# Performance work log

Measured on AMD Instinct MI355X. Metric: run time of the kernel, lower is better.

Reference implementation:

```python
import jax, jax.numpy as jnp
import numpy as np

LN_EPS = 1e-5

def _layernorm(x, gamma, beta):
    # LayerNorm over last axis
    mu = jnp.mean(x, axis=-1, keepdims=True)
    var = jnp.var(x, axis=-1, keepdims=True)
    return (x - mu) * jax.lax.rsqrt(var + LN_EPS) * gamma + beta

def setup_inputs() -> dict:
    key = jax.random.key(0)
    ks = jax.random.split(key, 5)
    N, M, d, K = 65536, 2048, 256, 512
    return {
        "H_rna": jax.random.normal(ks[0], (N, d), jnp.float32),
        "H_drug": jax.random.normal(ks[1], (M, d), jnp.float32),
        "U": jax.random.normal(ks[2], (d, K), jnp.float32),
        "V": jax.random.normal(ks[3], (K, d), jnp.float32),
        "q": jax.random.normal(ks[4], (K,), jnp.float32),
        "g_rna": jnp.ones((K,), jnp.float32),
        "b_rna": jnp.zeros((K,), jnp.float32),
        "g_drug": jnp.ones((K,), jnp.float32),
        "b_drug": jnp.zeros((K,), jnp.float32),
    }

def reference(H_rna, H_drug, U, V, q, g_rna, b_rna, g_drug, b_drug):
    # RNA branch: the torch code repeats H_rna over num_drug then projects;
    # all num_drug copies are identical, so compute once per RNA row.
    A = jnp.tanh(H_rna @ U)                    # [N, K]
    A = _layernorm(A, g_rna, b_rna)            # LN over K
    A = A * q                                  # elementwise gate
    # Drug branch: tanh(V @ H_drug^T) -> LN over K (applied on transposed view)
    Dp = jnp.tanh(V @ H_drug.T)                # [K, M]
    Dp = _layernorm(Dp.T, g_drug, b_drug).T    # LN over K axis -> [K, M]
    # Attention scores; identical across the repeated num_drug dim, so the
    # softmax+matmul+mean collapses exactly to a single [N, M] softmax.
    S = A @ Dp                                 # [N, M]
    P = jax.nn.softmax(S, axis=-1)             # [N, M]
    return P @ H_drug                          # [N, d]
```

## Files before the change

kernel.cpp:

```cpp
#include <hip/hip_runtime.h>
#include <math.h>

#define LN_EPS 1e-5f

typedef _Float16 h8 __attribute__((ext_vector_type(8)));
typedef _Float16 h4 __attribute__((ext_vector_type(4)));
typedef float f32x4 __attribute__((ext_vector_type(4)));

#define MFMA16(A,B,C) __builtin_amdgcn_mfma_f32_16x16x32_f16(A,B,C,0,0,0)

__device__ __forceinline__ float fast_tanh(float x){
    float e = __expf(2.f*x);
    return 1.f - 2.f/(e+1.f);
}

__global__ __launch_bounds__(512) void dp_kernel(
    const float* __restrict__ V, const float* __restrict__ Hd,
    const float* __restrict__ gd, const float* __restrict__ bd,
    _Float16* __restrict__ dp_pack)
{
    __shared__ float h_sh[4][256];
    __shared__ float red1[4][8];
    __shared__ float red2[4][8];

    const int t  = threadIdx.x;
    const int m0 = blockIdx.x * 4;

    for (int i = t; i < 4 * 256; i += 512)
        ((float*)h_sh)[i] = Hd[(size_t)m0 * 256 + i];
    __syncthreads();

    const int k = t;
    float x0 = 0.f, x1 = 0.f, x2 = 0.f, x3 = 0.f;
    for (int j = 0; j < 256; j += 4) {
        float4 v4 = *(const float4*)(V + (size_t)k * 256 + j);
        x0 += v4.x * h_sh[0][j] + v4.y * h_sh[0][j + 1] + v4.z * h_sh[0][j + 2] + v4.w * h_sh[0][j + 3];
        x1 += v4.x * h_sh[1][j] + v4.y * h_sh[1][j + 1] + v4.z * h_sh[1][j + 2] + v4.w * h_sh[1][j + 3];
        x2 += v4.x * h_sh[2][j] + v4.y * h_sh[2][j + 1] + v4.z * h_sh[2][j + 2] + v4.w * h_sh[2][j + 3];
        x3 += v4.x * h_sh[3][j] + v4.y * h_sh[3][j + 1] + v4.z * h_sh[3][j + 2] + v4.w * h_sh[3][j + 3];
    }
    float th[4];
    th[0] = tanhf(x0); th[1] = tanhf(x1); th[2] = tanhf(x2); th[3] = tanhf(x3);

    float s1[4], s2[4];
#pragma unroll
    for (int mi = 0; mi < 4; ++mi) { s1[mi] = th[mi]; s2[mi] = th[mi] * th[mi]; }
#pragma unroll
    for (int off = 32; off > 0; off >>= 1) {
#pragma unroll
        for (int mi = 0; mi < 4; ++mi) {
            s1[mi] += __shfl_xor(s1[mi], off, 64);
            s2[mi] += __shfl_xor(s2[mi], off, 64);
        }
    }
    const int wave = t >> 6;
    if ((t & 63) == 0) {
#pragma unroll
        for (int mi = 0; mi < 4; ++mi) { red1[mi][wave] = s1[mi]; red2[mi][wave] = s2[mi]; }
    }
    __syncthreads();

    const float gk = gd[k];
    const float bk = bd[k];
#pragma unroll
    for (int mi = 0; mi < 4; ++mi) {
        float sa = 0.f, sb = 0.f;
#pragma unroll
        for (int ww = 0; ww < 8; ++ww) { sa += red1[mi][ww]; sb += red2[mi][ww]; }
        float mu  = sa * (1.f / 512.f);
        float var = sb * (1.f / 512.f) - mu * mu;
        float rs  = rsqrtf(var + LN_EPS);
        float a   = (th[mi] - mu) * rs * gk + bk;
        int m  = m0 + mi;
        int mt = m >> 4, kk = k >> 5, ln = (m & 15) + 16 * ((k >> 3) & 3), j = k & 7;
        dp_pack[(size_t)((mt * 16 + kk) * 64 + ln) * 8 + j] = (_Float16)a;
    }
}

__global__ void pack_hd_kernel(const float* __restrict__ Hd, _Float16* __restrict__ hp)
{
    int m = blockIdx.x, c = threadIdx.x;
    float v = Hd[(size_t)m * 256 + c];
    int nt = c >> 4, kk = m >> 5, ln = (c & 15) + 16 * ((m >> 3) & 3), j = m & 7;
    hp[(size_t)((nt * 64 + kk) * 64 + ln) * 8 + j] = (_Float16)v;
}

__global__ void pack_u_kernel(const float* __restrict__ U,
                              _Float16* __restrict__ uh, _Float16* __restrict__ ul)
{
    int jd = blockIdx.x, n = threadIdx.x;
    float v = U[(size_t)jd * 512 + n];
    _Float16 hi = (_Float16)v;
    _Float16 lo = (_Float16)(v - (float)hi);
    int nt = n >> 4, kd = jd >> 5, ln = (n & 15) + 16 * ((jd >> 3) & 3), jj = jd & 7;
    int idx = ((nt * 8 + kd) * 64 + ln) * 8 + jj;
    uh[idx] = hi; ul[idx] = lo;
}

__global__ __launch_bounds__(512) void attn_kernel(
    const float* __restrict__ Hr, const float* __restrict__ q,
    const float* __restrict__ gr, const float* __restrict__ br,
    const _Float16* __restrict__ u_hi, const _Float16* __restrict__ u_lo,
    const _Float16* __restrict__ dp_pack, const _Float16* __restrict__ hd_pack,
    float* __restrict__ out)
{
    __shared__ __align__(16) _Float16 lds0[32768];
    __shared__ __align__(16) _Float16 p_pack[2][16384];
    __shared__ __align__(16) float stats[2][2][64][8];

    const int t    = threadIdx.x;
    const int w    = t >> 6;
    const int lane = t & 63;
    const int q4   = lane >> 4;
    const int l15  = lane & 15;
    const int blk  = blockIdx.x;

    _Float16* hr_hi  = lds0;
    _Float16* hr_lo  = lds0 + 16384;
    _Float16* a_pack = lds0;

    float gq[4], bq[4];
#pragma unroll
    for (int i = 0; i < 4; ++i) {
        int c = w * 64 + 16 * i + l15;
        gq[i] = gr[c] * q[c];
        bq[i] = br[c] * q[c];
    }

    const float* HrB = Hr + (size_t)blk * 64 * 256;
#pragma unroll
    for (int ii = 0; ii < 8; ++ii) {
        int flat = (t + 512 * ii) * 4;
        int r = flat >> 8, c = flat & 255;
        f32x4 v = __builtin_nontemporal_load((const f32x4*)(HrB + flat));
        int base = (((r >> 4) * 8 + (c >> 5)) * 64 + ((r & 15) + 16 * ((c >> 3) & 3))) * 8 + (c & 7);
        h4 hi, lo;
        hi[0] = (_Float16)v[0]; lo[0] = (_Float16)(v[0] - (float)hi[0]);
        hi[1] = (_Float16)v[1]; lo[1] = (_Float16)(v[1] - (float)hi[1]);
        hi[2] = (_Float16)v[2]; lo[2] = (_Float16)(v[2] - (float)hi[2]);
        hi[3] = (_Float16)v[3]; lo[3] = (_Float16)(v[3] - (float)hi[3]);
        *(h4*)(hr_hi + base) = hi;
        *(h4*)(hr_lo + base) = lo;
    }
    __syncthreads();

    f32x4 x[4][4];
#pragma unroll
    for (int rt = 0; rt < 4; ++rt)
#pragma unroll
        for (int ci = 0; ci < 4; ++ci) x[rt][ci] = (f32x4)(0.f);

#pragma unroll
    for (int kd = 0; kd < 8; ++kd) {
        h8 ah[4], al[4];
#pragma unroll
        for (int rt = 0; rt < 4; ++rt) {
            int idx = ((rt * 8 + kd) * 64 + lane) * 8;
            ah[rt] = *(h8*)(hr_hi + idx);
            al[rt] = *(h8*)(hr_lo + idx);
        }
        h8 bh[4], bl[4];
#pragma unroll
        for (int ci = 0; ci < 4; ++ci) {
            int idx = (((w * 4 + ci) * 8 + kd) * 64 + lane) * 8;
            bh[ci] = *(const h8*)(u_hi + idx);
            bl[ci] = *(const h8*)(u_lo + idx);
        }
#pragma unroll
        for (int rt = 0; rt < 4; ++rt)
#pragma unroll
            for (int ci = 0; ci < 4; ++ci) x[rt][ci] = MFMA16(ah[rt], bh[ci], x[rt][ci]);
#pragma unroll
        for (int rt = 0; rt < 4; ++rt)
#pragma unroll
            for (int ci = 0; ci < 4; ++ci) x[rt][ci] = MFMA16(ah[rt], bl[ci], x[rt][ci]);
#pragma unroll
        for (int rt = 0; rt < 4; ++rt)
#pragma unroll
            for (int ci = 0; ci < 4; ++ci) x[rt][ci] = MFMA16(al[rt], bh[ci], x[rt][ci]);
    }

    float s1[4][4], s2[4][4];
#pragma unroll
    for (int rt = 0; rt < 4; ++rt)
#pragma unroll
        for (int e = 0; e < 4; ++e) { s1[rt][e] = 0.f; s2[rt][e] = 0.f; }
#pragma unroll
    for (int rt = 0; rt < 4; ++rt)
#pragma unroll
        for (int ci = 0; ci < 4; ++ci)
#pragma unroll
            for (int e = 0; e < 4; ++e) {
                float th = fast_tanh(x[rt][ci][e]);
                x[rt][ci][e] = th;
                s1[rt][e] += th;
                s2[rt][e] += th * th;
            }
#pragma unroll
    for (int off = 1; off < 16; off <<= 1)
#pragma unroll
        for (int rt = 0; rt < 4; ++rt)
#pragma unroll
            for (int e = 0; e < 4; ++e) {
                s1[rt][e] += __shfl_xor(s1[rt][e], off, 64);
                s2[rt][e] += __shfl_xor(s2[rt][e], off, 64);
            }
    if (l15 == 0) {
#pragma unroll
        for (int rt = 0; rt < 4; ++rt)
#pragma unroll
            for (int e = 0; e < 4; ++e) {
                int row = rt * 16 + q4 * 4 + e;
                stats[0][0][row][w] = s1[rt][e];
                stats[0][1][row][w] = s2[rt][e];
            }
    }
    __syncthreads();

    float mu[4][4], rs_[4][4];
#pragma unroll
    for (int rt = 0; rt < 4; ++rt)
#pragma unroll
        for (int e = 0; e < 4; ++e) {
            int row = rt * 16 + q4 * 4 + e;
            f32x4 v1 = *(f32x4*)&stats[0][0][row][0];
            f32x4 v1b = *(f32x4*)&stats[0][0][row][4];
            f32x4 v2 = *(f32x4*)&stats[0][1][row][0];
            f32x4 v2b = *(f32x4*)&stats[0][1][row][4];
            float S1 = v1[0] + v1[1] + v1[2] + v1[3] + v1b[0] + v1b[1] + v1b[2] + v1b[3];
            float S2 = v2[0] + v2[1] + v2[2] + v2[3] + v2b[0] + v2b[1] + v2b[2] + v2b[3];
            float m  = S1 * (1.f / 512.f);
            float va = S2 * (1.f / 512.f) - m * m;
            mu[rt][e]  = m;
            rs_[rt][e] = rsqrtf(va + LN_EPS);
        }

#pragma unroll
    for (int rt = 0; rt < 4; ++rt)
#pragma unroll
        for (int ci = 0; ci < 4; ++ci)
#pragma unroll
            for (int e = 0; e < 4; ++e) {
                int mrow = q4 * 4 + e;
                int c = w * 64 + 16 * ci + l15;
                float a = (x[rt][ci][e] - mu[rt][e]) * rs_[rt][e] * gq[ci] + bq[ci];
                a_pack[((rt * 16 + (c >> 5)) * 64 + (mrow + 16 * ((c >> 3) & 3))) * 8 + (c & 7)] =
                    (_Float16)a;
            }
    __syncthreads();

    f32x4 o[4][2];
#pragma unroll
    for (int rt = 0; rt < 4; ++rt)
#pragma unroll
        for (int nc = 0; nc < 2; ++nc) o[rt][nc] = (f32x4)(0.f);
    float mrun[4][4], lrun[4][4];
#pragma unroll
    for (int rt = 0; rt < 4; ++rt)
#pragma unroll
        for (int e = 0; e < 4; ++e) { mrun[rt][e] = -3.0e38f; lrun[rt][e] = 0.f; }

    for (int it = 0; it < 8; ++it) {
        const int pb = it & 1;
        f32x4 s[4][2];
#pragma unroll
        for (int rt = 0; rt < 4; ++rt)
#pragma unroll
            for (int ct = 0; ct < 2; ++ct) s[rt][ct] = (f32x4)(0.f);
#pragma unroll
        for (int kk = 0; kk < 16; ++kk) {
            h8 af[4];
#pragma unroll
            for (int rt = 0; rt < 4; ++rt)
                af[rt] = *(h8*)(a_pack + ((rt * 16 + kk) * 64 + lane) * 8);
            h8 bf[2];
#pragma unroll
            for (int ct = 0; ct < 2; ++ct) {
                int mt = it * 16 + w * 2 + ct;
                bf[ct] = *(const h8*)(dp_pack + (size_t)((mt * 16 + kk) * 64 + lane) * 8);
            }
#pragma unroll
            for (int rt = 0; rt < 4; ++rt)
#pragma unroll
                for (int ct = 0; ct < 2; ++ct) s[rt][ct] = MFMA16(af[rt], bf[ct], s[rt][ct]);
        }

        float pm[4][4];
#pragma unroll
        for (int rt = 0; rt < 4; ++rt)
#pragma unroll
            for (int e = 0; e < 4; ++e)
                pm[rt][e] = fmaxf(s[rt][0][e], s[rt][1][e]);
#pragma unroll
        for (int off = 1; off < 16; off <<= 1)
#pragma unroll
            for (int rt = 0; rt < 4; ++rt)
#pragma unroll
                for (int e = 0; e < 4; ++e)
                    pm[rt][e] = fmaxf(pm[rt][e], __shfl_xor(pm[rt][e], off, 64));
        if (l15 == 0) {
#pragma unroll
            for (int rt = 0; rt < 4; ++rt)
#pragma unroll
                for (int e = 0; e < 4; ++e)
                    stats[pb][0][rt * 16 + q4 * 4 + e][w] = pm[rt][e];
        }
        __syncthreads();

        float alpha[4][4], mnew[4][4], psum[4][4];
#pragma unroll
        for (int rt = 0; rt < 4; ++rt)
#pragma unroll
            for (int e = 0; e < 4; ++e) {
                int row = rt * 16 + q4 * 4 + e;
                f32x4 v = *(f32x4*)&stats[pb][0][row][0];
                f32x4 vb = *(f32x4*)&stats[pb][0][row][4];
                float mn = fmaxf(fmaxf(fmaxf(v[0], v[1]), fmaxf(v[2], v[3])),
                                 fmaxf(fmaxf(vb[0], vb[1]), fmaxf(vb[2], vb[3])));
                mn = fmaxf(mn, mrun[rt][e]);
                alpha[rt][e] = __expf(mrun[rt][e] - mn);
                mnew[rt][e]  = mn;
                psum[rt][e]  = 0.f;
            }
#pragma unroll
        for (int rt = 0; rt < 4; ++rt)
#pragma unroll
            for (int ct = 0; ct < 2; ++ct)
#pragma unroll
                for (int e = 0; e < 4; ++e) {
                    float p = __expf(s[rt][ct][e] - mnew[rt][e]);
                    s[rt][ct][e] = p;
                    psum[rt][e] += p;
                }
#pragma unroll
        for (int off = 1; off < 16; off <<= 1)
#pragma unroll
            for (int rt = 0; rt < 4; ++rt)
#pragma unroll
                for (int e = 0; e < 4; ++e)
                    psum[rt][e] += __shfl_xor(psum[rt][e], off, 64);
        if (l15 == 0) {
#pragma unroll
            for (int rt = 0; rt < 4; ++rt)
#pragma unroll
                for (int e = 0; e < 4; ++e)
                    stats[pb][1][rt * 16 + q4 * 4 + e][w] = psum[rt][e];
        }
#pragma unroll
        for (int rt = 0; rt < 4; ++rt)
#pragma unroll
            for (int ct = 0; ct < 2; ++ct)
#pragma unroll
                for (int e = 0; e < 4; ++e) {
                    int mrow = q4 * 4 + e;
                    int col  = 32 * w + 16 * ct + l15;
                    p_pack[pb][((rt * 8 + (col >> 5)) * 64 + (mrow + 16 * ((col >> 3) & 3))) * 8 + (col & 7)] =
                        (_Float16)s[rt][ct][e];
                }
#pragma unroll
        for (int rt = 0; rt < 4; ++rt)
#pragma unroll
            for (int nc = 0; nc < 2; ++nc)
#pragma unroll
                for (int e = 0; e < 4; ++e) o[rt][nc][e] *= alpha[rt][e];
        __syncthreads();

#pragma unroll
        for (int rt = 0; rt < 4; ++rt)
#pragma unroll
            for (int e = 0; e < 4; ++e) {
                int row = rt * 16 + q4 * 4 + e;
                f32x4 v = *(f32x4*)&stats[pb][1][row][0];
                f32x4 vb = *(f32x4*)&stats[pb][1][row][4];
                lrun[rt][e] = lrun[rt][e] * alpha[rt][e] +
                              (v[0] + v[1] + v[2] + v[3] + vb[0] + vb[1] + vb[2] + vb[3]);
                mrun[rt][e] = mnew[rt][e];
            }

#pragma unroll
        for (int kp = 0; kp < 8; ++kp) {
            h8 pf[4];
#pragma unroll
            for (int rt = 0; rt < 4; ++rt)
                pf[rt] = *(h8*)(&p_pack[pb][((rt * 8 + kp) * 64 + lane) * 8]);
            h8 hf[2];
#pragma unroll
            for (int nc = 0; nc < 2; ++nc) {
                int nt = 2 * w + nc;
                hf[nc] = *(const h8*)(hd_pack + (size_t)((nt * 64 + it * 8 + kp) * 64 + lane) * 8);
            }
#pragma unroll
            for (int rt = 0; rt < 4; ++rt)
#pragma unroll
                for (int nc = 0; nc < 2; ++nc) o[rt][nc] = MFMA16(pf[rt], hf[nc], o[rt][nc]);
        }
    }

    float inv[4][4];
#pragma unroll
    for (int rt = 0; rt < 4; ++rt)
#pragma unroll
        for (int e = 0; e < 4; ++e) inv[rt][e] = 1.f / lrun[rt][e];
#pragma unroll
    for (int rt = 0; rt < 4; ++rt)
#pragma unroll
        for (int nc = 0; nc < 2; ++nc)
#pragma unroll
            for (int e = 0; e < 4; ++e) {
                int row = rt * 16 + q4 * 4 + e;
                int c   = (2 * w + nc) * 16 + l15;
                out[((size_t)blk * 64 + row) * 256 + c] = o[rt][nc][e] * inv[rt][e];
            }
}

extern "C" void kernel_launch(void* const* d_in, const int* in_sizes, int n_in,
                              void* d_out, int out_size, void* d_ws, size_t ws_size,
                              hipStream_t stream)
{
    const float* Hr = (const float*)d_in[0];
    const float* Hd = (const float*)d_in[1];
    const float* U  = (const float*)d_in[2];
    const float* V  = (const float*)d_in[3];
    const float* q  = (const float*)d_in[4];
    const float* gr = (const float*)d_in[5];
    const float* br = (const float*)d_in[6];
    const float* gd = (const float*)d_in[7];
    const float* bd = (const float*)d_in[8];
    float* out = (float*)d_out;

    const int N = in_sizes[0] / 256;
    const int M = in_sizes[1] / 256;

    char* ws = (char*)d_ws;
    _Float16* dp_pack = (_Float16*)ws;
    _Float16* hd_pack = (_Float16*)(ws + (2u << 20));
    _Float16* u_hi    = (_Float16*)(ws + (3u << 20));
    _Float16* u_lo    = (_Float16*)(ws + (3u << 20) + (256u << 10));

    dp_kernel<<<dim3(M / 4), dim3(512), 0, stream>>>(V, Hd, gd, bd, dp_pack);
    pack_hd_kernel<<<dim3(M), dim3(256), 0, stream>>>(Hd, hd_pack);
    pack_u_kernel<<<dim3(256), dim3(512), 0, stream>>>(U, u_hi, u_lo);
    attn_kernel<<<dim3(N / 64), dim3(512), 0, stream>>>(Hr, q, gr, br, u_hi, u_lo,
                                                        dp_pack, hd_pack, out);
}
```

Measured before the change: 688.1 us.

## Give each wave its own row tile in flash attention loop, drop block syncs

Each block now handles 128 RNA rows in two passes of the U projection and LayerNorm stage. In the attention loop each wave owns 16 rows with its A fragments held in registers, streams all drug columns itself and keeps a private P tile in LDS. This removes the per-iteration block-wide max/sum reductions and __syncthreads. It also adds lazy softmax rescaling (rescale only when the running max grows by more than 8) and register double-buffering of dp_pack loads. The cost is more registers (16 output accumulators plus 16 A fragments), more LDS, and each wave reading all of dp_pack and hd_pack from global memory, which lowers operand reuse across waves.

Result: slower. 1.243 ms (+80.7%).

```diff
diff --git a/kernel.cpp b/kernel.cpp
--- a/kernel.cpp
+++ b/kernel.cpp
@@ -104,9 +104,9 @@
     const _Float16* __restrict__ dp_pack, const _Float16* __restrict__ hd_pack,
     float* __restrict__ out)
 {
-    __shared__ __align__(16) _Float16 lds0[32768];
-    __shared__ __align__(16) _Float16 p_pack[2][16384];
-    __shared__ __align__(16) float stats[2][2][64][8];
+    __shared__ __align__(16) _Float16 lds0[65536];
+    __shared__ __align__(16) _Float16 p_lds[8192];
+    __shared__ __align__(16) float stats[2][64][8];
 
     const int t    = threadIdx.x;
     const int w    = t >> 6;
@@ -115,8 +115,8 @@
     const int l15  = lane & 15;
     const int blk  = blockIdx.x;
 
-    _Float16* hr_hi  = lds0;
-    _Float16* hr_lo  = lds0 + 16384;
+    _Float16* hr_hi  = lds0 + 32768;
+    _Float16* hr_lo  = lds0 + 49152;
     _Float16* a_pack = lds0;
 
     float gq[4], bq[4];
@@ -127,290 +127,239 @@
         bq[i] = br[c] * q[c];
     }
 
-    const float* HrB = Hr + (size_t)blk * 64 * 256;
-#pragma unroll
-    for (int ii = 0; ii < 8; ++ii) {
-        int flat = (t + 512 * ii) * 4;
-        int r = flat >> 8, c = flat & 255;
-        f32x4 v = __builtin_nontemporal_load((const f32x4*)(HrB + flat));
-        int base = (((r >> 4) * 8 + (c >> 5)) * 64 + ((r & 15) + 16 * ((c >> 3) & 3))) * 8 + (c & 7);
-        h4 hi, lo;
-        hi[0] = (_Float16)v[0]; lo[0] = (_Float16)(v[0] - (float)hi[0]);
-        hi[1] = (_Float16)v[1]; lo[1] = (_Float16)(v[1] - (float)hi[1]);
-        hi[2] = (_Float16)v[2]; lo[2] = (_Float16)(v[2] - (float)hi[2]);
-        hi[3] = (_Float16)v[3]; lo[3] = (_Float16)(v[3] - (float)hi[3]);
-        *(h4*)(hr_hi + base) = hi;
-        *(h4*)(hr_lo + base) = lo;
-    }
-    __syncthreads();
-
-    f32x4 x[4][4];
-#pragma unroll
-    for (int rt = 0; rt < 4; ++rt)
-#pragma unroll
-        for (int ci = 0; ci < 4; ++ci) x[rt][ci] = (f32x4)(0.f);
-
-#pragma unroll
-    for (int kd = 0; kd < 8; ++kd) {
-        h8 ah[4], al[4];
-#pragma unroll
-        for (int rt = 0; rt < 4; ++rt) {
-            int idx = ((rt * 8 + kd) * 64 + lane) * 8;
-            ah[rt] = *(h8*)(hr_hi + idx);
-            al[rt] = *(h8*)(hr_lo + idx);
-        }
-        h8 bh[4], bl[4];
-#pragma unroll
-        for (int ci = 0; ci < 4; ++ci) {
-            int idx = (((w * 4 + ci) * 8 + kd) * 64 + lane) * 8;
-            bh[ci] = *(const h8*)(u_hi + idx);
-            bl[ci] = *(const h8*)(u_lo + idx);
-        }
-#pragma unroll
-        for (int rt = 0; rt < 4; ++rt)
-#pragma unroll
-            for (int ci = 0; ci < 4; ++ci) x[rt][ci] = MFMA16(ah[rt], bh[ci], x[rt][ci]);
-#pragma unroll
-        for (int rt = 0; rt < 4; ++rt)
-#pragma unroll
-            for (int ci = 0; ci < 4; ++ci) x[rt][ci] = MFMA16(ah[rt], bl[ci], x[rt][ci]);
-#pragma unroll
-        for (int rt = 0; rt < 4; ++rt)
-#pragma unroll
-            for (int ci = 0; ci < 4; ++ci) x[rt][ci] = MFMA16(al[rt], bh[ci], x[rt][ci]);
-    }
-
-    float s1[4][4], s2[4][4];
-#pragma unroll
-    for (int rt = 0; rt < 4; ++rt)
-#pragma unroll
-        for (int e = 0; e < 4; ++e) { s1[rt][e] = 0.f; s2[rt][e] = 0.f; }
-#pragma unroll
-    for (int rt = 0; rt < 4; ++rt)
-#pragma unroll
-        for (int ci = 0; ci < 4; ++ci)
-#pragma unroll
-            for (int e = 0; e < 4; ++e) {
-                float th = fast_tanh(x[rt][ci][e]);
-                x[rt][ci][e] = th;
-                s1[rt][e] += th;
-                s2[rt][e] += th * th;
-            }
-#pragma unroll
-    for (int off = 1; off < 16; off <<= 1)
-#pragma unroll
-        for (int rt = 0; rt < 4; ++rt)
-#pragma unroll
-            for (int e = 0; e < 4; ++e) {
-                s1[rt][e] += __shfl_xor(s1[rt][e], off, 64);
-                s2[rt][e] += __shfl_xor(s2[rt][e], off, 64);
-            }
-    if (l15 == 0) {
+    for (int pass = 0; pass < 2; ++pass) {
+        const float* HrB = Hr + ((size_t)blk * 128 + pass * 64) * 256;
+#pragma unroll
+        for (int ii = 0; ii < 8; ++ii) {
+            int flat = (t + 512 * ii) * 4;
+            int r = flat >> 8, c = flat & 255;
+            f32x4 v = __builtin_nontemporal_load((const f32x4*)(HrB + flat));
+            int base = (((r >> 4) * 8 + (c >> 5)) * 64 + ((r & 15) + 16 * ((c >> 3) & 3))) * 8 + (c & 7);
+            h4 hi, lo;
+            hi[0] = (_Float16)v[0]; lo[0] = (_Float16)(v[0] - (float)hi[0]);
+            hi[1] = (_Float16)v[1]; lo[1] = (_Float16)(v[1] - (float)hi[1]);
+            hi[2] = (_Float16)v[2]; lo[2] = (_Float16)(v[2] - (float)hi[2]);
+            hi[3] = (_Float16)v[3]; lo[3] = (_Float16)(v[3] - (float)hi[3]);
+            *(h4*)(hr_hi + base) = hi;
+            *(h4*)(hr_lo + base) = lo;
+        }
+        __syncthreads();
+
+        f32x4 x[4][4];
+#pragma unroll
+        for (int rt = 0; rt < 4; ++rt)
+#pragma unroll
+            for (int ci = 0; ci < 4; ++ci) x[rt][ci] = (f32x4)(0.f);
+
+#pragma unroll
+        for (int kd = 0; kd < 8; ++kd) {
+            h8 ah[4], al[4];
+#pragma unroll
+            for (int rt = 0; rt < 4; ++rt) {
+                int idx = ((rt * 8 + kd) * 64 + lane) * 8;
+                ah[rt] = *(h8*)(hr_hi + idx);
+                al[rt] = *(h8*)(hr_lo + idx);
+            }
+            h8 bh[4], bl[4];
+#pragma unroll
+            for (int ci = 0; ci < 4; ++ci) {
+                int idx = (((w * 4 + ci) * 8 + kd) * 64 + lane) * 8;
+                bh[ci] = *(const h8*)(u_hi + idx);
+                bl[ci] = *(const h8*)(u_lo + idx);
+            }
+#pragma unroll
+            for (int rt = 0; rt < 4; ++rt)
+#pragma unroll
+                for (int ci = 0; ci < 4; ++ci) x[rt][ci] = MFMA16(ah[rt], bh[ci], x[rt][ci]);
+#pragma unroll
+            for (int rt = 0; rt < 4; ++rt)
+#pragma unroll
+                for (int ci = 0; ci < 4; ++ci) x[rt][ci] = MFMA16(ah[rt], bl[ci], x[rt][ci]);
+#pragma unroll
+            for (int rt = 0; rt < 4; ++rt)
+#pragma unroll
+                for (int ci = 0; ci < 4; ++ci) x[rt][ci] = MFMA16(al[rt], bh[ci], x[rt][ci]);
+        }
+
+        float s1[4][4], s2[4][4];
+#pragma unroll
+        for (int rt = 0; rt < 4; ++rt)
+#pragma unroll
+            for (int e = 0; e < 4; ++e) { s1[rt][e] = 0.f; s2[rt][e] = 0.f; }
+#pragma unroll
+        for (int rt = 0; rt < 4; ++rt)
+#pragma unroll
+            for (int ci = 0; ci < 4; ++ci)
+#pragma unroll
+                for (int e = 0; e < 4; ++e) {
+                    float th = fast_tanh(x[rt][ci][e]);
+                    x[rt][ci][e] = th;
+                    s1[rt][e] += th;
+                    s2[rt][e] += th * th;
+                }
+#pragma unroll
+        for (int off = 1; off < 16; off <<= 1)
+#pragma unroll
+            for (int rt = 0; rt < 4; ++rt)
+#pragma unroll
+                for (int e = 0; e < 4; ++e) {
+                    s1[rt][e] += __shfl_xor(s1[rt][e], off, 64);
+                    s2[rt][e] += __shfl_xor(s2[rt][e], off, 64);
+                }
+        if (l15 == 0) {
+#pragma unroll
+            for (int rt = 0; rt < 4; ++rt)
+#pragma unroll
+                for (int e = 0; e < 4; ++e) {
+                    int row = rt * 16 + q4 * 4 + e;
+                    stats[0][row][w] = s1[rt][e];
+                    stats[1][row][w] = s2[rt][e];
+                }
+        }
+        __syncthreads();
+
+        float mu[4][4], rs_[4][4];
 #pragma unroll
         for (int rt = 0; rt < 4; ++rt)
 #pragma unroll
             for (int e = 0; e < 4; ++e) {
                 int row = rt * 16 + q4 * 4 + e;
-                stats[0][0][row][w] = s1[rt][e];
-                stats[0][1][row][w] = s2[rt][e];
-            }
-    }
-    __syncthreads();
-
-    float mu[4][4], rs_[4][4];
-#pragma unroll
-    for (int rt = 0; rt < 4; ++rt)
-#pragma unroll
-        for (int e = 0; e < 4; ++e) {
-            int row = rt * 16 + q4 * 4 + e;
-            f32x4 v1 = *(f32x4*)&stats[0][0][row][0];
-            f32x4 v1b = *(f32x4*)&stats[0][0][row][4];
-            f32x4 v2 = *(f32x4*)&stats[0][1][row][0];
-            f32x4 v2b = *(f32x4*)&stats[0][1][row][4];
-            float S1 = v1[0] + v1[1] + v1[2] + v1[3] + v1b[0] + v1b[1] + v1b[2] + v1b[3];
-            float S2 = v2[0] + v2[1] + v2[2] + v2[3] + v2b[0] + v2b[1] + v2b[2] + v2b[3];
-            float m  = S1 * (1.f / 512.f);
-            float va = S2 * (1.f / 512.f) - m * m;
-            mu[rt][e]  = m;
-            rs_[rt][e] = rsqrtf(va + LN_EPS);
-        }
-
-#pragma unroll
-    for (int rt = 0; rt < 4; ++rt)
-#pragma unroll
-        for (int ci = 0; ci < 4; ++ci)
-#pragma unroll
-            for (int e = 0; e < 4; ++e) {
-                int mrow = q4 * 4 + e;
-                int c = w * 64 + 16 * ci + l15;
-                float a = (x[rt][ci][e] - mu[rt][e]) * rs_[rt][e] * gq[ci] + bq[ci];
-                a_pack[((rt * 16 + (c >> 5)) * 64 + (mrow + 16 * ((c >> 3) & 3))) * 8 + (c & 7)] =
-                    (_Float16)a;
-            }
-    __syncthreads();
-
-    f32x4 o[4][2];
-#pragma unroll
-    for (int rt = 0; rt < 4; ++rt)
-#pragma unroll
-        for (int nc = 0; nc < 2; ++nc) o[rt][nc] = (f32x4)(0.f);
-    float mrun[4][4], lrun[4][4];
-#pragma unroll
-    for (int rt = 0; rt < 4; ++rt)
-#pragma unroll
-        for (int e = 0; e < 4; ++e) { mrun[rt][e] = -3.0e38f; lrun[rt][e] = 0.f; }
-
-    for (int it = 0; it < 8; ++it) {
-        const int pb = it & 1;
-        f32x4 s[4][2];
-#pragma unroll
-        for (int rt = 0; rt < 4; ++rt)
-#pragma unroll
-            for (int ct = 0; ct < 2; ++ct) s[rt][ct] = (f32x4)(0.f);
-#pragma unroll
-        for (int kk = 0; kk < 16; ++kk) {
-            h8 af[4];
-#pragma unroll
-            for (int rt = 0; rt < 4; ++rt)
-                af[rt] = *(h8*)(a_pack + ((rt * 16 + kk) * 64 + lane) * 8);
-            h8 bf[2];
-#pragma unroll
-            for (int ct = 0; ct < 2; ++ct) {
-                int mt = it * 16 + w * 2 + ct;
-                bf[ct] = *(const h8*)(dp_pack + (size_t)((mt * 16 + kk) * 64 + lane) * 8);
-            }
-#pragma unroll
-            for (int rt = 0; rt < 4; ++rt)
-#pragma unroll
-                for (int ct = 0; ct < 2; ++ct) s[rt][ct] = MFMA16(af[rt], bf[ct], s[rt][ct]);
-        }
-
-        float pm[4][4];
-#pragma unroll
-        for (int rt = 0; rt < 4; ++rt)
-#pragma unroll
-            for (int e = 0; e < 4; ++e)
-                pm[rt][e] = fmaxf(s[rt][0][e], s[rt][1][e]);
-#pragma unroll
-        for (int off = 1; off < 16; off <<= 1)
-#pragma unroll
-            for (int rt = 0; rt < 4; ++rt)
-#pragma unroll
-                for (int e = 0; e < 4; ++e)
-                    pm[rt][e] = fmaxf(pm[rt][e], __shfl_xor(pm[rt][e], off, 64));
-        if (l15 == 0) {
-#pragma unroll
-            for (int rt = 0; rt < 4; ++rt)
-#pragma unroll
-                for (int e = 0; e < 4; ++e)
-                    stats[pb][0][rt * 16 + q4 * 4 + e][w] = pm[rt][e];
-        }
-        __syncthreads();
-
-        float alpha[4][4], mnew[4][4], psum[4][4];
-#pragma unroll
-        for (int rt = 0; rt < 4; ++rt)
-#pragma unroll
-            for (int e = 0; e < 4; ++e) {
-                int row = rt * 16 + q4 * 4 + e;
-                f32x4 v = *(f32x4*)&stats[pb][0][row][0];
-                f32x4 vb = *(f32x4*)&stats[pb][0][row][4];
-                float mn = fmaxf(fmaxf(fmaxf(v[0], v[1]), fmaxf(v[2], v[3])),
-                                 fmaxf(fmaxf(vb[0], vb[1]), fmaxf(vb[2], vb[3])));
-                mn = fmaxf(mn, mrun[rt][e]);
-                alpha[rt][e] = __expf(mrun[rt][e] - mn);
-                mnew[rt][e]  = mn;
-                psum[rt][e]  = 0.f;
-            }
-#pragma unroll
-        for (int rt = 0; rt < 4; ++rt)
-#pragma unroll
-            for (int ct = 0; ct < 2; ++ct)
-#pragma unroll
-                for (int e = 0; e < 4; ++e) {
-                    float p = __expf(s[rt][ct][e] - mnew[rt][e]);
-                    s[rt][ct][e] = p;
-                    psum[rt][e] += p;
-                }
-#pragma unroll
-        for (int off = 1; off < 16; off <<= 1)
-#pragma unroll
-            for (int rt = 0; rt < 4; ++rt)
-#pragma unroll
-                for (int e = 0; e < 4; ++e)
-                    psum[rt][e] += __shfl_xor(psum[rt][e], off, 64);
-        if (l15 == 0) {
-#pragma unroll
-            for (int rt = 0; rt < 4; ++rt)
-#pragma unroll
-                for (int e = 0; e < 4; ++e)
-                    stats[pb][1][rt * 16 + q4 * 4 + e][w] = psum[rt][e];
-        }
-#pragma unroll
-        for (int rt = 0; rt < 4; ++rt)
-#pragma unroll
-            for (int ct = 0; ct < 2; ++ct)
+                f32x4 v1  = *(f32x4*)&stats[0][row][0];
+                f32x4 v1b = *(f32x4*)&stats[0][row][4];
+                f32x4 v2  = *(f32x4*)&stats[1][row][0];
+                f32x4 v2b = *(f32x4*)&stats[1][row][4];
+                float S1 = v1[0]+v1[1]+v1[2]+v1[3]+v1b[0]+v1b[1]+v1b[2]+v1b[3];
+                float S2 = v2[0]+v2[1]+v2[2]+v2[3]+v2b[0]+v2b[1]+v2b[2]+v2b[3];
+                float m  = S1 * (1.f / 512.f);
+                float va = S2 * (1.f / 512.f) - m * m;
+                mu[rt][e]  = m;
+                rs_[rt][e] = rsqrtf(va + LN_EPS);
+            }
+
+#pragma unroll
+        for (int rt = 0; rt < 4; ++rt)
+#pragma unroll
+            for (int ci = 0; ci < 4; ++ci)
 #pragma unroll
                 for (int e = 0; e < 4; ++e) {
                     int mrow = q4 * 4 + e;
-                    int col  = 32 * w + 16 * ct + l15;
-                    p_pack[pb][((rt * 8 + (col >> 5)) * 64 + (mrow + 16 * ((col >> 3) & 3))) * 8 + (col & 7)] =
-                        (_Float16)s[rt][ct][e];
-                }
-#pragma unroll
-        for (int rt = 0; rt < 4; ++rt)
-#pragma unroll
-            for (int nc = 0; nc < 2; ++nc)
-#pragma unroll
-                for (int e = 0; e < 4; ++e) o[rt][nc][e] *= alpha[rt][e];
-        __syncthreads();
-
-#pragma unroll
-        for (int rt = 0; rt < 4; ++rt)
+                    int c = w * 64 + 16 * ci + l15;
+                    float a = (x[rt][ci][e] - mu[rt][e]) * rs_[rt][e] * gq[ci] + bq[ci];
+                    a_pack[(((pass * 4 + rt) * 16 + (c >> 5)) * 64 + (mrow + 16 * ((c >> 3) & 3))) * 8 + (c & 7)] =
+                        (_Float16)a;
+                }
+    }
+    __syncthreads();
+
+    h8 a[16];
+#pragma unroll
+    for (int kk = 0; kk < 16; ++kk)
+        a[kk] = *(h8*)(a_pack + ((w * 16 + kk) * 64 + lane) * 8);
+
+    _Float16* pw = p_lds + w * 1024;
+
+    f32x4 o[16];
+#pragma unroll
+    for (int ct = 0; ct < 16; ++ct) o[ct] = (f32x4)(0.f);
+    float m_[4], l_[4];
+#pragma unroll
+    for (int e = 0; e < 4; ++e) { m_[e] = -3.0e38f; l_[e] = 0.f; }
+
+    for (int itc = 0; itc < 32; ++itc) {
+        f32x4 s[4];
+#pragma unroll
+        for (int ct2 = 0; ct2 < 4; ++ct2) s[ct2] = (f32x4)(0.f);
+
+        h8 bfa[4], bfb[4];
+#pragma unroll
+        for (int ct2 = 0; ct2 < 4; ++ct2)
+            bfa[ct2] = *(const h8*)(dp_pack + (size_t)(((itc * 4 + ct2) * 16 + 0) * 64 + lane) * 8);
+#pragma unroll
+        for (int kk = 0; kk < 16; ++kk) {
+            if (kk + 1 < 16) {
+#pragma unroll
+                for (int ct2 = 0; ct2 < 4; ++ct2) {
+                    h8 v = *(const h8*)(dp_pack + (size_t)(((itc * 4 + ct2) * 16 + (kk + 1)) * 64 + lane) * 8);
+                    if (kk & 1) bfa[ct2] = v; else bfb[ct2] = v;
+                }
+            }
+#pragma unroll
+            for (int ct2 = 0; ct2 < 4; ++ct2) {
+                h8 cur = (kk & 1) ? bfb[ct2] : bfa[ct2];
+                s[ct2] = MFMA16(a[kk], cur, s[ct2]);
+            }
+        }
+
+        float pm[4];
+#pragma unroll
+        for (int e = 0; e < 4; ++e)
+            pm[e] = fmaxf(fmaxf(s[0][e], s[1][e]), fmaxf(s[2][e], s[3][e]));
+#pragma unroll
+        for (int off = 1; off < 16; off <<= 1)
+#pragma unroll
+            for (int e = 0; e < 4; ++e)
+                pm[e] = fmaxf(pm[e], __shfl_xor(pm[e], off, 64));
+
+        float grow = fmaxf(fmaxf(pm[0] - m_[0], pm[1] - m_[1]),
+                           fmaxf(pm[2] - m_[2], pm[3] - m_[3]));
+        if (__any(grow > 8.f)) {
 #pragma unroll
             for (int e = 0; e < 4; ++e) {
-                int row = rt * 16 + q4 * 4 + e;
-                f32x4 v = *(f32x4*)&stats[pb][1][row][0];
-                f32x4 vb = *(f32x4*)&stats[pb][1][row][4];
-                lrun[rt][e] = lrun[rt][e] * alpha[rt][e] +
-                              (v[0] + v[1] + v[2] + v[3] + vb[0] + vb[1] + vb[2] + vb[3]);
-                mrun[rt][e] = mnew[rt][e];
-            }
-
-#pragma unroll
-        for (int kp = 0; kp < 8; ++kp) {
-            h8 pf[4];
-#pragma unroll
-            for (int rt = 0; rt < 4; ++rt)
-                pf[rt] = *(h8*)(&p_pack[pb][((rt * 8 + kp) * 64 + lane) * 8]);
-            h8 hf[2];
-#pragma unroll
-            for (int nc = 0; nc < 2; ++nc) {
-                int nt = 2 * w + nc;
-                hf[nc] = *(const h8*)(hd_pack + (size_t)((nt * 64 + it * 8 + kp) * 64 + lane) * 8);
-            }
-#pragma unroll
-            for (int rt = 0; rt < 4; ++rt)
-#pragma unroll
-                for (int nc = 0; nc < 2; ++nc) o[rt][nc] = MFMA16(pf[rt], hf[nc], o[rt][nc]);
-        }
-    }
-
-    float inv[4][4];
-#pragma unroll
-    for (int rt = 0; rt < 4; ++rt)
-#pragma unroll
-        for (int e = 0; e < 4; ++e) inv[rt][e] = 1.f / lrun[rt][e];
-#pragma unroll
-    for (int rt = 0; rt < 4; ++rt)
-#pragma unroll
-        for (int nc = 0; nc < 2; ++nc)
+                float mn = fmaxf(m_[e], pm[e]);
+                float al = __expf(m_[e] - mn);
+                m_[e] = mn;
+                l_[e] *= al;
+#pragma unroll
+                for (int ct = 0; ct < 16; ++ct) o[ct][e] *= al;
+            }
+        }
+#pragma unroll
+        for (int ct2 = 0; ct2 < 4; ++ct2)
 #pragma unroll
             for (int e = 0; e < 4; ++e) {
-                int row = rt * 16 + q4 * 4 + e;
-                int c   = (2 * w + nc) * 16 + l15;
-                out[((size_t)blk * 64 + row) * 256 + c] = o[rt][nc][e] * inv[rt][e];
-            }
+                float p = __expf(s[ct2][e] - m_[e]);
+                s[ct2][e] = p;
+                l_[e] += p;
+            }
+#pragma unroll
+        for (int ct2 = 0; ct2 < 4; ++ct2)
+#pragma unroll
+            for (int e = 0; e < 4; ++e) {
+                int c = 16 * ct2 + l15;
+                int row = 4 * q4 + e;
+                pw[((c >> 5) * 64 + ((c >> 3) & 3) * 16 + row) * 8 + (c & 7)] = (_Float16)s[ct2][e];
+            }
+        h8 pf0 = *(h8*)(pw + (0 * 64 + lane) * 8);
+        h8 pf1 = *(h8*)(pw + (1 * 64 + lane) * 8);
+
+#pragma unroll
+        for (int ct = 0; ct < 16; ++ct) {
+            h8 hf = *(const h8*)(hd_pack + (size_t)((ct * 64 + itc * 2 + 0) * 64 + lane) * 8);
+            o[ct] = MFMA16(pf0, hf, o[ct]);
+        }
+#pragma unroll
+        for (int ct = 0; ct < 16; ++ct) {
+            h8 hf = *(const h8*)(hd_pack + (size_t)((ct * 64 + itc * 2 + 1) * 64 + lane) * 8);
+            o[ct] = MFMA16(pf1, hf, o[ct]);
+        }
+    }
+
+#pragma unroll
+    for (int off = 1; off < 16; off <<= 1)
+#pragma unroll
+        for (int e = 0; e < 4; ++e)
+            l_[e] += __shfl_xor(l_[e], off, 64);
+    float inv[4];
+#pragma unroll
+    for (int e = 0; e < 4; ++e) inv[e] = 1.f / l_[e];
+
+#pragma unroll
+    for (int ct = 0; ct < 16; ++ct)
+#pragma unroll
+        for (int e = 0; e < 4; ++e) {
+            int row = w * 16 + 4 * q4 + e;
+            out[((size_t)blk * 128 + row) * 256 + 16 * ct + l15] = o[ct][e] * inv[e];
+        }
 }
 
 extern "C" void kernel_launch(void* const* d_in, const int* in_sizes, int n_in,
@@ -440,6 +389,6 @@
     dp_kernel<<<dim3(M / 4), dim3(512), 0, stream>>>(V, Hd, gd, bd, dp_pack);
     pack_hd_kernel<<<dim3(M), dim3(256), 0, stream>>>(Hd, hd_pack);
     pack_u_kernel<<<dim3(256), dim3(512), 0, stream>>>(U, u_hi, u_lo);
-    attn_kernel<<<dim3(N / 64), dim3(512), 0, stream>>>(Hr, q, gr, br, u_hi, u_lo,
-                                                        dp_pack, hd_pack, out);
-}
+    attn_kernel<<<dim3(N / 128), dim3(512), 0, stream>>>(Hr, q, gr, br, u_hi, u_lo,
+                                                         dp_pack, hd_pack, out);
+}
```

## Software-pipeline attention loop: compute next score tile before current PV, defer row-sum reduction

Applied to the files above, without the earlier changes.

Restructures the online-softmax loop so the QK^T MFMAs for the next block of drug columns run before the softmax and PV product of the current block. The row-max cross-wave exchange then needs only one barrier per iteration. Each thread keeps its own partial row sums, which are reduced across waves once at the end instead of every iteration. It also raises wave priority around the MFMA sections with s_setprio. The aim is to cut barriers and overlap matrix work with exp/shuffle work, at the cost of more live registers for the extra score tile, which may reduce occupancy.

Measured after the change: 715.3 us. 3.9% more time.

```diff
diff --git a/kernel.cpp b/kernel.cpp
--- a/kernel.cpp
+++ b/kernel.cpp
@@ -106,7 +106,7 @@
 {
     __shared__ __align__(16) _Float16 lds0[32768];
     __shared__ __align__(16) _Float16 p_pack[2][16384];
-    __shared__ __align__(16) float stats[2][2][64][8];
+    __shared__ __align__(16) float smax[2][64][8];
 
     const int t    = threadIdx.x;
     const int w    = t >> 6;
@@ -166,6 +166,7 @@
             bh[ci] = *(const h8*)(u_hi + idx);
             bl[ci] = *(const h8*)(u_lo + idx);
         }
+        __builtin_amdgcn_s_setprio(1);
 #pragma unroll
         for (int rt = 0; rt < 4; ++rt)
 #pragma unroll
@@ -178,6 +179,7 @@
         for (int rt = 0; rt < 4; ++rt)
 #pragma unroll
             for (int ci = 0; ci < 4; ++ci) x[rt][ci] = MFMA16(al[rt], bh[ci], x[rt][ci]);
+        __builtin_amdgcn_s_setprio(0);
     }
 
     float s1[4][4], s2[4][4];
@@ -211,8 +213,8 @@
 #pragma unroll
             for (int e = 0; e < 4; ++e) {
                 int row = rt * 16 + q4 * 4 + e;
-                stats[0][0][row][w] = s1[rt][e];
-                stats[0][1][row][w] = s2[rt][e];
+                smax[0][row][w] = s1[rt][e];
+                smax[1][row][w] = s2[rt][e];
             }
     }
     __syncthreads();
@@ -223,12 +225,12 @@
 #pragma unroll
         for (int e = 0; e < 4; ++e) {
             int row = rt * 16 + q4 * 4 + e;
-            f32x4 v1 = *(f32x4*)&stats[0][0][row][0];
-            f32x4 v1b = *(f32x4*)&stats[0][0][row][4];
-            f32x4 v2 = *(f32x4*)&stats[0][1][row][0];
-            f32x4 v2b = *(f32x4*)&stats[0][1][row][4];
-            float S1 = v1[0] + v1[1] + v1[2] + v1[3] + v1b[0] + v1b[1] + v1b[2] + v1b[3];
-            float S2 = v2[0] + v2[1] + v2[2] + v2[3] + v2b[0] + v2b[1] + v2b[2] + v2b[3];
+            f32x4 v1  = *(f32x4*)&smax[0][row][0];
+            f32x4 v1b = *(f32x4*)&smax[0][row][4];
+            f32x4 v2  = *(f32x4*)&smax[1][row][0];
+            f32x4 v2b = *(f32x4*)&smax[1][row][4];
+            float S1 = v1[0]+v1[1]+v1[2]+v1[3]+v1b[0]+v1b[1]+v1b[2]+v1b[3];
+            float S2 = v2[0]+v2[1]+v2[2]+v2[3]+v2b[0]+v2b[1]+v2b[2]+v2b[3];
             float m  = S1 * (1.f / 512.f);
             float va = S2 * (1.f / 512.f) - m * m;
             mu[rt][e]  = m;
@@ -260,13 +262,14 @@
 #pragma unroll
         for (int e = 0; e < 4; ++e) { mrun[rt][e] = -3.0e38f; lrun[rt][e] = 0.f; }
 
-    for (int it = 0; it < 8; ++it) {
-        const int pb = it & 1;
-        f32x4 s[4][2];
-#pragma unroll
-        for (int rt = 0; rt < 4; ++rt)
-#pragma unroll
-            for (int ct = 0; ct < 2; ++ct) s[rt][ct] = (f32x4)(0.f);
+    f32x4 sprev[4][2];
+
+    {
+#pragma unroll
+        for (int rt = 0; rt < 4; ++rt)
+#pragma unroll
+            for (int ct = 0; ct < 2; ++ct) sprev[rt][ct] = (f32x4)(0.f);
+        __builtin_amdgcn_s_setprio(1);
 #pragma unroll
         for (int kk = 0; kk < 16; ++kk) {
             h8 af[4];
@@ -276,21 +279,22 @@
             h8 bf[2];
 #pragma unroll
             for (int ct = 0; ct < 2; ++ct) {
-                int mt = it * 16 + w * 2 + ct;
+                int mt = w * 2 + ct;
                 bf[ct] = *(const h8*)(dp_pack + (size_t)((mt * 16 + kk) * 64 + lane) * 8);
             }
 #pragma unroll
             for (int rt = 0; rt < 4; ++rt)
 #pragma unroll
-                for (int ct = 0; ct < 2; ++ct) s[rt][ct] = MFMA16(af[rt], bf[ct], s[rt][ct]);
-        }
+                for (int ct = 0; ct < 2; ++ct) sprev[rt][ct] = MFMA16(af[rt], bf[ct], sprev[rt][ct]);
+        }
+        __builtin_amdgcn_s_setprio(0);
 
         float pm[4][4];
 #pragma unroll
         for (int rt = 0; rt < 4; ++rt)
 #pragma unroll
             for (int e = 0; e < 4; ++e)
-                pm[rt][e] = fmaxf(s[rt][0][e], s[rt][1][e]);
+                pm[rt][e] = fmaxf(sprev[rt][0][e], sprev[rt][1][e]);
 #pragma unroll
         for (int off = 1; off < 16; off <<= 1)
 #pragma unroll
@@ -303,49 +307,75 @@
             for (int rt = 0; rt < 4; ++rt)
 #pragma unroll
                 for (int e = 0; e < 4; ++e)
-                    stats[pb][0][rt * 16 + q4 * 4 + e][w] = pm[rt][e];
-        }
-        __syncthreads();
-
-        float alpha[4][4], mnew[4][4], psum[4][4];
+                    smax[0][rt * 16 + q4 * 4 + e][w] = pm[rt][e];
+        }
+    }
+    __syncthreads();
+
+    for (int it = 1; it <= 8; ++it) {
+        const int pb = (it - 1) & 1;
+
+        f32x4 scur[4][2];
+        if (it < 8) {
+#pragma unroll
+            for (int rt = 0; rt < 4; ++rt)
+#pragma unroll
+                for (int ct = 0; ct < 2; ++ct) scur[rt][ct] = (f32x4)(0.f);
+            __builtin_amdgcn_s_setprio(1);
+#pragma unroll
+            for (int kk = 0; kk < 16; ++kk) {
+                h8 af[4];
+#pragma unroll
+                for (int rt = 0; rt < 4; ++rt)
+                    af[rt] = *(h8*)(a_pack + ((rt * 16 + kk) * 64 + lane) * 8);
+                h8 bf[2];
+#pragma unroll
+                for (int ct = 0; ct < 2; ++ct) {
+                    int mt = it * 16 + w * 2 + ct;
+                    bf[ct] = *(const h8*)(dp_pack + (size_t)((mt * 16 + kk) * 64 + lane) * 8);
+                }
+#pragma unroll
+                for (int rt = 0; rt < 4; ++rt)
+#pragma unroll
+                    for (int ct = 0; ct < 2; ++ct) scur[rt][ct] = MFMA16(af[rt], bf[ct], scur[rt][ct]);
+            }
+            __builtin_amdgcn_s_setprio(0);
+        }
+
+        float alpha[4][4];
 #pragma unroll
         for (int rt = 0; rt < 4; ++rt)
 #pragma unroll
             for (int e = 0; e < 4; ++e) {
                 int row = rt * 16 + q4 * 4 + e;
-                f32x4 v = *(f32x4*)&stats[pb][0][row][0];
-                f32x4 vb = *(f32x4*)&stats[pb][0][row][4];
-                float mn = fmaxf(fmaxf(fmaxf(v[0], v[1]), fmaxf(v[2], v[3])),
-                                 fmaxf(fmaxf(vb[0], vb[1]), fmaxf(vb[2], vb[3])));
-                mn = fmaxf(mn, mrun[rt][e]);
+                f32x4 v  = *(f32x4*)&smax[pb][row][0];
+                f32x4 vb = *(f32x4*)&smax[pb][row][4];
+                float g = fmaxf(fmaxf(fmaxf(v[0], v[1]), fmaxf(v[2], v[3])),
+                                fmaxf(fmaxf(vb[0], vb[1]), fmaxf(vb[2], vb[3])));
+                float mn = fmaxf(mrun[rt][e], g);
                 alpha[rt][e] = __expf(mrun[rt][e] - mn);
-                mnew[rt][e]  = mn;
-                psum[rt][e]  = 0.f;
-            }
+                mrun[rt][e]  = mn;
+            }
+        float psum[4][4];
+#pragma unroll
+        for (int rt = 0; rt < 4; ++rt)
+#pragma unroll
+            for (int e = 0; e < 4; ++e) psum[rt][e] = 0.f;
 #pragma unroll
         for (int rt = 0; rt < 4; ++rt)
 #pragma unroll
             for (int ct = 0; ct < 2; ++ct)
 #pragma unroll
                 for (int e = 0; e < 4; ++e) {
-                    float p = __expf(s[rt][ct][e] - mnew[rt][e]);
-                    s[rt][ct][e] = p;
+                    float p = __expf(sprev[rt][ct][e] - mrun[rt][e]);
+                    sprev[rt][ct][e] = p;
                     psum[rt][e] += p;
                 }
 #pragma unroll
-        for (int off = 1; off < 16; off <<= 1)
-#pragma unroll
-            for (int rt = 0; rt < 4; ++rt)
-#pragma unroll
-                for (int e = 0; e < 4; ++e)
-                    psum[rt][e] += __shfl_xor(psum[rt][e], off, 64);
-        if (l15 == 0) {
-#pragma unroll
-            for (int rt = 0; rt < 4; ++rt)
-#pragma unroll
-                for (int e = 0; e < 4; ++e)
-                    stats[pb][1][rt * 16 + q4 * 4 + e][w] = psum[rt][e];
-        }
+        for (int rt = 0; rt < 4; ++rt)
+#pragma unroll
+            for (int e = 0; e < 4; ++e)
+                lrun[rt][e] = lrun[rt][e] * alpha[rt][e] + psum[rt][e];
 #pragma unroll
         for (int rt = 0; rt < 4; ++rt)
 #pragma unroll
@@ -355,7 +385,7 @@
                     int mrow = q4 * 4 + e;
                     int col  = 32 * w + 16 * ct + l15;
                     p_pack[pb][((rt * 8 + (col >> 5)) * 64 + (mrow + 16 * ((col >> 3) & 3))) * 8 + (col & 7)] =
-                        (_Float16)s[rt][ct][e];
+                        (_Float16)sprev[rt][ct][e];
                 }
 #pragma unroll
         for (int rt = 0; rt < 4; ++rt)
@@ -363,20 +393,33 @@
             for (int nc = 0; nc < 2; ++nc)
 #pragma unroll
                 for (int e = 0; e < 4; ++e) o[rt][nc][e] *= alpha[rt][e];
+
+        if (it < 8) {
+            float pm[4][4];
+#pragma unroll
+            for (int rt = 0; rt < 4; ++rt)
+#pragma unroll
+                for (int e = 0; e < 4; ++e)
+                    pm[rt][e] = fmaxf(scur[rt][0][e], scur[rt][1][e]);
+#pragma unroll
+            for (int off = 1; off < 16; off <<= 1)
+#pragma unroll
+                for (int rt = 0; rt < 4; ++rt)
+#pragma unroll
+                    for (int e = 0; e < 4; ++e)
+                        pm[rt][e] = fmaxf(pm[rt][e], __shfl_xor(pm[rt][e], off, 64));
+            if (l15 == 0) {
+#pragma unroll
+                for (int rt = 0; rt < 4; ++rt)
+#pragma unroll
+                    for (int e = 0; e < 4; ++e)
+                        smax[it & 1][rt * 16 + q4 * 4 + e][w] = pm[rt][e];
+            }
+        }
+
         __syncthreads();
 
-#pragma unroll
-        for (int rt = 0; rt < 4; ++rt)
-#pragma unroll
-            for (int e = 0; e < 4; ++e) {
-                int row = rt * 16 + q4 * 4 + e;
-                f32x4 v = *(f32x4*)&stats[pb][1][row][0];
-                f32x4 vb = *(f32x4*)&stats[pb][1][row][4];
-                lrun[rt][e] = lrun[rt][e] * alpha[rt][e] +
-                              (v[0] + v[1] + v[2] + v[3] + vb[0] + vb[1] + vb[2] + vb[3]);
-                mrun[rt][e] = mnew[rt][e];
-            }
-
+        __builtin_amdgcn_s_setprio(1);
 #pragma unroll
         for (int kp = 0; kp < 8; ++kp) {
             h8 pf[4];
@@ -387,20 +430,50 @@
 #pragma unroll
             for (int nc = 0; nc < 2; ++nc) {
                 int nt = 2 * w + nc;
-                hf[nc] = *(const h8*)(hd_pack + (size_t)((nt * 64 + it * 8 + kp) * 64 + lane) * 8);
+                hf[nc] = *(const h8*)(hd_pack + (size_t)((nt * 64 + (it - 1) * 8 + kp) * 64 + lane) * 8);
             }
 #pragma unroll
             for (int rt = 0; rt < 4; ++rt)
 #pragma unroll
                 for (int nc = 0; nc < 2; ++nc) o[rt][nc] = MFMA16(pf[rt], hf[nc], o[rt][nc]);
         }
-    }
+        __builtin_amdgcn_s_setprio(0);
+
+        if (it < 8) {
+#pragma unroll
+            for (int rt = 0; rt < 4; ++rt)
+#pragma unroll
+                for (int ct = 0; ct < 2; ++ct) sprev[rt][ct] = scur[rt][ct];
+        }
+    }
+
+#pragma unroll
+    for (int off = 1; off < 16; off <<= 1)
+#pragma unroll
+        for (int rt = 0; rt < 4; ++rt)
+#pragma unroll
+            for (int e = 0; e < 4; ++e)
+                lrun[rt][e] += __shfl_xor(lrun[rt][e], off, 64);
+    if (l15 == 0) {
+#pragma unroll
+        for (int rt = 0; rt < 4; ++rt)
+#pragma unroll
+            for (int e = 0; e < 4; ++e)
+                smax[0][rt * 16 + q4 * 4 + e][w] = lrun[rt][e];
+    }
+    __syncthreads();
 
     float inv[4][4];
 #pragma unroll
     for (int rt = 0; rt < 4; ++rt)
 #pragma unroll
-        for (int e = 0; e < 4; ++e) inv[rt][e] = 1.f / lrun[rt][e];
+        for (int e = 0; e < 4; ++e) {
+            int row = rt * 16 + q4 * 4 + e;
+            f32x4 v  = *(f32x4*)&smax[0][row][0];
+            f32x4 vb = *(f32x4*)&smax[0][row][4];
+            float l = v[0]+v[1]+v[2]+v[3]+vb[0]+vb[1]+vb[2]+vb[3];
+            inv[rt][e] = 1.f / l;
+        }
 #pragma unroll
     for (int rt = 0; rt < 4; ++rt)
 #pragma unroll
```
